# Optimization experiments

Hardware: AMD Instinct MI355X
Metric: run time of the kernel (lower is better)

The kernel has to match this reference:

```python
import jax, jax.numpy as jnp
import numpy as np

B, L, H = 32, 512, 1024
H2 = H // 2          # split half = 512
D_ATTN = 64
EPS = 1e-5


def setup_inputs() -> dict:
    key = jax.random.key(0)
    ks = jax.random.split(key, 6)
    x = jax.random.normal(ks[0], (B, L, H), dtype=jnp.float32)
    # LayerNorm params (default torch init: weight=1, bias=0)
    ln_gamma = jnp.ones((H2,), jnp.float32)
    ln_beta = jnp.zeros((H2,), jnp.float32)
    # Toeplitz params (module inits w_vector=0, bias=1; use small random w for nontrivial math)
    w_vector = jax.random.normal(ks[1], (2 * L - 1,), jnp.float32) * 0.02
    t_bias = jnp.ones((L,), jnp.float32)
    # TinyAttention: kqv Linear(H2 -> 3*d_attn), proj Linear(d_attn -> H2)
    kqv_w = jax.random.normal(ks[2], (H2, 3 * D_ATTN), jnp.float32) * 0.02
    kqv_b = jnp.zeros((3 * D_ATTN,), jnp.float32)
    proj_w = jax.random.normal(ks[3], (D_ATTN, H2), jnp.float32) * 0.02
    proj_b = jnp.zeros((H2,), jnp.float32)
    return {"x": x, "ln_gamma": ln_gamma, "ln_beta": ln_beta,
            "w_vector": w_vector, "t_bias": t_bias,
            "kqv_w": kqv_w, "kqv_b": kqv_b, "proj_w": proj_w, "proj_b": proj_b}


def _toeplitz(w_vector):
    # Faithful replication of get_toeplitz(): pad, tile, trim, reshape, crop.
    r = w_vector.shape[0] // 2            # = L - 1
    t = jnp.pad(w_vector, (0, L))         # length 3L - 1
    t = jnp.tile(t, L)[:-L]               # length L * (3L - 2)
    t = t.reshape(L, 3 * L - 2)
    return t[:, r:-r]                      # [L, L]


def _tiny_attention(v, kqv_w, kqv_b, proj_w, proj_b):
    kqv = v @ kqv_w + kqv_b                        # [B, L, 3*d_attn]
    k, q, val = jnp.split(kqv, 3, axis=-1)         # chunk order: key, query, value
    scale = 1.0 / jnp.sqrt(jnp.float32(q.shape[-1]))
    scores = jnp.einsum('bqd,bkd->bqk', q, k) * scale
    soft = jax.nn.softmax(scores, axis=-1)
    head = jnp.einsum('bqk,bkd->bqd', soft, val)   # [B, L, d_attn]
    return head @ proj_w + proj_b                  # [B, L, H2]


def reference(x, ln_gamma, ln_beta, w_vector, t_bias, kqv_w, kqv_b, proj_w, proj_b):
    u, v = jnp.split(x, 2, axis=-1)                # each [B, L, H2]
    head = _tiny_attention(v, kqv_w, kqv_b, proj_w, proj_b)
    # LayerNorm over last dim
    mu = jnp.mean(v, axis=-1, keepdims=True)
    var = jnp.mean(jnp.square(v - mu), axis=-1, keepdims=True)
    vn = (v - mu) * jax.lax.rsqrt(var + EPS) * ln_gamma + ln_beta
    # spatial (Toeplitz) mixing: permute -> [B, H2, L], matmul [L, L], bias
    w_t = _toeplitz(w_vector)
    vm = jnp.einsum('blc,lm->bmc', vn, w_t.T).transpose(0, 2, 1)  # keep faithful: vp @ w_t
    vm = jnp.einsum('bcl,lm->bcm', vn.transpose(0, 2, 1), w_t) + t_bias
    v_out = vm.transpose(0, 2, 1) + head           # [B, L, H2]
    return u * v_out
```

## Files before the change

kernel.cpp:

```cpp
#include <hip/hip_runtime.h>
#include <math.h>

#define NB 32
#define LL 512
#define HH 1024
#define H2 512
#define DA 64

typedef unsigned int u32;
typedef unsigned short u16;
typedef __bf16 bf16x8 __attribute__((ext_vector_type(8)));
typedef float f32x4 __attribute__((ext_vector_type(4)));

__device__ __forceinline__ u16 f2bu(float f) {
    u32 u = __builtin_bit_cast(u32, f);
    u = (u + 0x7fff + ((u >> 16) & 1)) >> 16;
    return (u16)u;
}

__device__ __forceinline__ void async_cp16(const void* g, void* l) {
    __builtin_amdgcn_global_load_lds(
        (const __attribute__((address_space(1))) u32*)g,
        (__attribute__((address_space(3))) u32*)l, 16, 0, 0);
}

__global__ void prep_kernel(const float* __restrict__ wv,
                            const float* __restrict__ kqvw,
                            const float* __restrict__ projw,
                            u16* __restrict__ wt, u16* __restrict__ kqvwT,
                            u16* __restrict__ projwT) {
    int e = blockIdx.x * 256 + threadIdx.x;
    if (e < 262144) {
        int m = e >> 9, l = e & 511;
        wt[e] = f2bu(wv[511 + m - l]);
    } else if (e < 262144 + 98304) {
        int i = e - 262144;
        int n = i >> 9, k = i & 511;
        kqvwT[i] = f2bu(kqvw[(size_t)k * 192 + n]);
    } else {
        int i = e - 360448;
        int c = i >> 6, d = i & 63;
        projwT[i] = f2bu(projw[(size_t)d * 512 + c]);
    }
}

__global__ void ln_kernel(const float* __restrict__ x,
                          const float* __restrict__ gamma,
                          const float* __restrict__ beta,
                          u16* __restrict__ vn) {
    int row = blockIdx.x;
    const float* vr = x + (size_t)row * HH + H2;
    int t = threadIdx.x;
    float a0 = vr[t], a1 = vr[t + 256];
    float s = a0 + a1, ss = a0 * a0 + a1 * a1;
#pragma unroll
    for (int off = 32; off > 0; off >>= 1) {
        s  += __shfl_down(s, off);
        ss += __shfl_down(ss, off);
    }
    __shared__ float ws[4], wss[4], stats[2];
    int wave = t >> 6;
    if ((t & 63) == 0) { ws[wave] = s; wss[wave] = ss; }
    __syncthreads();
    if (t == 0) {
        float S  = ws[0] + ws[1] + ws[2] + ws[3];
        float SS = wss[0] + wss[1] + wss[2] + wss[3];
        float mu  = S * (1.0f / H2);
        float var = SS * (1.0f / H2) - mu * mu;
        stats[0] = mu; stats[1] = rsqrtf(var + 1e-5f);
    }
    __syncthreads();
    float mu = stats[0], rstd = stats[1];
    u16* o = vn + (size_t)row * H2;
    o[t]       = f2bu((a0 - mu) * rstd * gamma[t]       + beta[t]);
    o[t + 256] = f2bu((a1 - mu) * rstd * gamma[t + 256] + beta[t + 256]);
}

__global__ void transpose_kernel(const u16* __restrict__ in, u16* __restrict__ outT) {
    __shared__ u16 T[64][65];
    int b = blockIdx.z, l0 = blockIdx.y * 64, c0 = blockIdx.x * 64;
    int t = threadIdx.x;
#pragma unroll
    for (int s = 0; s < 4; ++s) {
        int ci = t + s * 256;
        int row = ci >> 4, c4 = (ci & 15) * 4;
        ushort4 v = *(const ushort4*)(in + ((size_t)(b * LL + l0 + row)) * H2 + c0 + c4);
        T[c4 + 0][row] = v.x; T[c4 + 1][row] = v.y;
        T[c4 + 2][row] = v.z; T[c4 + 3][row] = v.w;
    }
    __syncthreads();
#pragma unroll
    for (int s = 0; s < 4; ++s) {
        int ci = t + s * 256;
        int c = ci >> 4, l4 = (ci & 15) * 4;
        ushort4 w;
        w.x = T[c][l4 + 0]; w.y = T[c][l4 + 1];
        w.z = T[c][l4 + 2]; w.w = T[c][l4 + 3];
        *(ushort4*)(outT + ((size_t)(b * H2 + c0 + c)) * LL + l0 + l4) = w;
    }
}

__global__ __launch_bounds__(256, 2)
void kqv_kernel(const float* __restrict__ x, const u16* __restrict__ wT,
                const float* __restrict__ bias,
                u16* __restrict__ qb, u16* __restrict__ kb, u16* __restrict__ vT) {
    __shared__ u16 smem[8192];
    u16* As = smem;
    u16* Bs = smem + 2048;
    int r0 = blockIdx.x * 64;
    int t = threadIdx.x, lane = t & 63, wid = t >> 6;
    int wm = (wid >> 1) * 32, wn = (wid & 1) * 96;
    int l15 = lane & 15, q16 = lane >> 4, q8 = q16 * 8;
    f32x4 acc[2][6] = {};
    for (int k0 = 0; k0 < 512; k0 += 32) {
#pragma unroll
        for (int s = 0; s < 3; ++s) {
            int ci = t + s * 256;
            async_cp16(wT + (size_t)(ci >> 2) * 512 + k0 + (ci & 3) * 8, Bs + ci * 8);
        }
#pragma unroll
        for (int s = 0; s < 2; ++s) {
            int ci = t + s * 256;
            int row = ci >> 3, c4 = (ci & 7) * 4;
            float4 v = *(const float4*)(x + (size_t)(r0 + row) * HH + H2 + k0 + c4);
            ushort4 p;
            p.x = f2bu(v.x); p.y = f2bu(v.y); p.z = f2bu(v.z); p.w = f2bu(v.w);
            *(ushort4*)(As + row * 32 + c4) = p;
        }
        __syncthreads();
        bf16x8 a[2], bb[6];
#pragma unroll
        for (int i = 0; i < 2; ++i)
            a[i] = *(const bf16x8*)(As + (wm + i * 16 + l15) * 32 + q8);
#pragma unroll
        for (int j = 0; j < 6; ++j)
            bb[j] = *(const bf16x8*)(Bs + (wn + j * 16 + l15) * 32 + q8);
#pragma unroll
        for (int i = 0; i < 2; ++i)
#pragma unroll
            for (int j = 0; j < 6; ++j)
                acc[i][j] = __builtin_amdgcn_mfma_f32_16x16x32_bf16(a[i], bb[j], acc[i][j], 0, 0, 0);
        __syncthreads();
    }
    u16* Ts = smem;
    int bb2 = r0 >> 9, l0loc = r0 & 511;
    int rq = q16 * 4;
#pragma unroll
    for (int i = 0; i < 2; ++i)
#pragma unroll
        for (int r = 0; r < 4; ++r) {
            int mloc = wm + i * 16 + rq + r;
            size_t mg = (size_t)(r0 + mloc);
#pragma unroll
            for (int j = 0; j < 6; ++j) {
                int n = wn + j * 16 + l15;
                u16 hv = f2bu(acc[i][j][r] + bias[n]);
                if (n < 64)       kb[mg * 64 + n] = hv;
                else if (n < 128) qb[mg * 64 + (n - 64)] = hv;
                else              Ts[(n - 128) * 68 + mloc] = hv;
            }
        }
    __syncthreads();
    int d = t >> 2, mo = (t & 3) * 16;
    u16* dst = vT + ((size_t)(bb2 * 64 + d)) * 512 + l0loc + mo;
    const u16* srcl = Ts + d * 68 + mo;
#pragma unroll
    for (int c = 0; c < 4; ++c)
        ((ushort4*)dst)[c] = ((const ushort4*)srcl)[c];
}

#define VLD 136
__global__ __launch_bounds__(256, 4)
void attn_kernel(const u16* __restrict__ qb, const u16* __restrict__ kb,
                 const u16* __restrict__ vT, u16* __restrict__ head) {
    __shared__ u16 Ps[4 * 16 * VLD];
    __shared__ float Osh[4][16 * 65];
    __shared__ float Msh[4][16], Lsh[4][16];
    int b = blockIdx.y, q0 = blockIdx.x * 16;
    int t = threadIdx.x, lane = t & 63, w = t >> 6;
    int l15 = lane & 15, q16 = lane >> 4, q8 = q16 * 8;
    int kc = w * 128;
    const u16* qg = qb + (size_t)b * LL * DA;
    const u16* kg = kb + (size_t)b * LL * DA;
    const u16* vg = vT + (size_t)b * DA * LL;

    bf16x8 aq[2];
#pragma unroll
    for (int s = 0; s < 2; ++s)
        aq[s] = *(const bf16x8*)(qg + (size_t)(q0 + l15) * DA + s * 32 + q8);

    f32x4 sc[8] = {};
#pragma unroll
    for (int j = 0; j < 8; ++j) {
#pragma unroll
        for (int s = 0; s < 2; ++s) {
            bf16x8 bk = *(const bf16x8*)(kg + (size_t)(kc + j * 16 + l15) * DA + s * 32 + q8);
            sc[j] = __builtin_amdgcn_mfma_f32_16x16x32_bf16(aq[s], bk, sc[j], 0, 0, 0);
        }
    }
    float mx[4], sm[4];
#pragma unroll
    for (int j = 0; j < 8; ++j)
#pragma unroll
        for (int r = 0; r < 4; ++r) sc[j][r] *= 0.125f;
#pragma unroll
    for (int r = 0; r < 4; ++r) {
        float m0 = sc[0][r];
#pragma unroll
        for (int j = 1; j < 8; ++j) m0 = fmaxf(m0, sc[j][r]);
        m0 = fmaxf(m0, __shfl_xor(m0, 1));
        m0 = fmaxf(m0, __shfl_xor(m0, 2));
        m0 = fmaxf(m0, __shfl_xor(m0, 4));
        m0 = fmaxf(m0, __shfl_xor(m0, 8));
        mx[r] = m0;
    }
#pragma unroll
    for (int j = 0; j < 8; ++j)
#pragma unroll
        for (int r = 0; r < 4; ++r) sc[j][r] = __expf(sc[j][r] - mx[r]);
#pragma unroll
    for (int r = 0; r < 4; ++r) {
        float s0 = sc[0][r];
#pragma unroll
        for (int j = 1; j < 8; ++j) s0 += sc[j][r];
        s0 += __shfl_xor(s0, 1);
        s0 += __shfl_xor(s0, 2);
        s0 += __shfl_xor(s0, 4);
        s0 += __shfl_xor(s0, 8);
        sm[r] = s0;
    }
    u16* Pw = Ps + w * 16 * VLD;
#pragma unroll
    for (int j = 0; j < 8; ++j)
#pragma unroll
        for (int r = 0; r < 4; ++r)
            Pw[(q16 * 4 + r) * VLD + j * 16 + l15] = f2bu(sc[j][r]);
    f32x4 o[4] = {};
#pragma unroll
    for (int kt = 0; kt < 4; ++kt) {
        bf16x8 ap = *(const bf16x8*)(Pw + l15 * VLD + kt * 32 + q8);
#pragma unroll
        for (int j = 0; j < 4; ++j) {
            bf16x8 bv = *(const bf16x8*)(vg + (size_t)(j * 16 + l15) * LL + kc + kt * 32 + q8);
            o[j] = __builtin_amdgcn_mfma_f32_16x16x32_bf16(ap, bv, o[j], 0, 0, 0);
        }
    }
#pragma unroll
    for (int j = 0; j < 4; ++j)
#pragma unroll
        for (int r = 0; r < 4; ++r)
            Osh[w][(q16 * 4 + r) * 65 + j * 16 + l15] = o[j][r];
    if (l15 == 0) {
#pragma unroll
        for (int r = 0; r < 4; ++r) {
            Msh[w][q16 * 4 + r] = mx[r];
            Lsh[w][q16 * 4 + r] = sm[r];
        }
    }
    __syncthreads();
    int q = t >> 4, dg = (t & 15) * 4;
    float m0 = Msh[0][q], m1 = Msh[1][q], m2 = Msh[2][q], m3 = Msh[3][q];
    float ms = fmaxf(fmaxf(m0, m1), fmaxf(m2, m3));
    float f0 = __expf(m0 - ms), f1 = __expf(m1 - ms), f2 = __expf(m2 - ms), f3 = __expf(m3 - ms);
    float lst = Lsh[0][q] * f0 + Lsh[1][q] * f1 + Lsh[2][q] * f2 + Lsh[3][q] * f3;
    float inv = 1.0f / lst;
    ushort4 res;
    u16* rp = (u16*)&res;
#pragma unroll
    for (int i = 0; i < 4; ++i) {
        int idx = q * 65 + dg + i;
        float a = Osh[0][idx] * f0 + Osh[1][idx] * f1 + Osh[2][idx] * f2 + Osh[3][idx] * f3;
        rp[i] = f2bu(a * inv);
    }
    *(ushort4*)(head + (size_t)(b * LL + q0 + q) * DA + dg) = res;
}

__device__ __forceinline__ void mfma_step(const u16* As, const u16* Bs,
                                          f32x4 acc[4][4], int wm, int wn, int lane) {
    int l15 = lane & 15, q8 = (lane >> 4) * 8;
    bf16x8 a[4], bv[4];
#pragma unroll
    for (int i = 0; i < 4; ++i)
        a[i] = *(const bf16x8*)(As + (wm + i * 16 + l15) * 32 + q8);
#pragma unroll
    for (int j = 0; j < 4; ++j)
        bv[j] = *(const bf16x8*)(Bs + (wn + j * 16 + l15) * 32 + q8);
#pragma unroll
    for (int i = 0; i < 4; ++i)
#pragma unroll
        for (int j = 0; j < 4; ++j)
            acc[i][j] = __builtin_amdgcn_mfma_f32_16x16x32_bf16(a[i], bv[j], acc[i][j], 0, 0, 0);
}

__global__ __launch_bounds__(256, 2)
void mix_kernel(const u16* __restrict__ wt,
                const u16* __restrict__ vnT,
                const u16* __restrict__ headb,
                const u16* __restrict__ projwT,
                const float* __restrict__ x,
                const float* __restrict__ tbias,
                const float* __restrict__ projb,
                float* __restrict__ out) {
    __shared__ u16 As[128 * 32];
    __shared__ u16 Bs[128 * 32];
    int b = blockIdx.z, m0 = blockIdx.y * 128, c0 = blockIdx.x * 128;
    int t = threadIdx.x, lane = t & 63, wid = t >> 6;
    int wm = (wid >> 1) * 64, wn = (wid & 1) * 64;
    f32x4 acc[4][4] = {};
    int ci0 = t, ci1 = t + 256;
    int r0a = ci0 >> 2, s0a = (ci0 & 3) * 8;
    int r1a = ci1 >> 2, s1a = (ci1 & 3) * 8;
    const u16* Ag = wt + (size_t)m0 * 512;
    const u16* Bg = vnT + ((size_t)b * H2 + c0) * 512;
    for (int k0 = 0; k0 < 512; k0 += 32) {
        async_cp16(Ag + (size_t)r0a * 512 + k0 + s0a, As + ci0 * 8);
        async_cp16(Ag + (size_t)r1a * 512 + k0 + s1a, As + ci1 * 8);
        async_cp16(Bg + (size_t)r0a * 512 + k0 + s0a, Bs + ci0 * 8);
        async_cp16(Bg + (size_t)r1a * 512 + k0 + s1a, Bs + ci1 * 8);
        __syncthreads();
        mfma_step(As, Bs, acc, wm, wn, lane);
        __syncthreads();
    }
    const u16* Hg = headb + ((size_t)b * LL + m0) * DA;
    const u16* Pg = projwT + (size_t)c0 * DA;
    for (int k0 = 0; k0 < 64; k0 += 32) {
        async_cp16(Hg + (size_t)r0a * 64 + k0 + s0a, As + ci0 * 8);
        async_cp16(Hg + (size_t)r1a * 64 + k0 + s1a, As + ci1 * 8);
        async_cp16(Pg + (size_t)r0a * 64 + k0 + s0a, Bs + ci0 * 8);
        async_cp16(Pg + (size_t)r1a * 64 + k0 + s1a, Bs + ci1 * 8);
        __syncthreads();
        mfma_step(As, Bs, acc, wm, wn, lane);
        __syncthreads();
    }
    int l15 = lane & 15, rq = (lane >> 4) * 4;
#pragma unroll
    for (int i = 0; i < 4; ++i) {
#pragma unroll
        for (int r = 0; r < 4; ++r) {
            int m = m0 + wm + i * 16 + rq + r;
            float tb = tbias[m];
            const float* xrow = x + ((size_t)b * LL + m) * HH;
            float* orow = out + ((size_t)b * LL + m) * H2;
#pragma unroll
            for (int j = 0; j < 4; ++j) {
                int c = c0 + wn + j * 16 + l15;
                float val = acc[i][j][r] + tb + projb[c];
                orow[c] = xrow[c] * val;
            }
        }
    }
}

extern "C" void kernel_launch(void* const* d_in, const int* in_sizes, int n_in,
                              void* d_out, int out_size, void* d_ws, size_t ws_size,
                              hipStream_t stream) {
    (void)in_sizes; (void)n_in; (void)out_size; (void)ws_size;
    const float* x     = (const float*)d_in[0];
    const float* gamma = (const float*)d_in[1];
    const float* beta  = (const float*)d_in[2];
    const float* wv    = (const float*)d_in[3];
    const float* tb    = (const float*)d_in[4];
    const float* kqvw  = (const float*)d_in[5];
    const float* kqvb  = (const float*)d_in[6];
    const float* projw = (const float*)d_in[7];
    const float* projb = (const float*)d_in[8];
    float* out = (float*)d_out;

    u16* vn_bf   = (u16*)d_ws;
    u16* vnT_bf  = vn_bf + (size_t)NB * LL * H2;
    u16* qb      = vnT_bf + (size_t)NB * LL * H2;
    u16* kb      = qb + (size_t)NB * LL * DA;
    u16* vTb     = kb + (size_t)NB * LL * DA;
    u16* head_bf = vTb + (size_t)NB * LL * DA;
    u16* wt_bf   = head_bf + (size_t)NB * LL * DA;
    u16* kqvwT   = wt_bf + 512 * 512;
    u16* projwT  = kqvwT + 192 * 512;

    prep_kernel     <<<1536, 256, 0, stream>>>(wv, kqvw, projw, wt_bf, kqvwT, projwT);
    ln_kernel       <<<NB * LL, 256, 0, stream>>>(x, gamma, beta, vn_bf);
    transpose_kernel<<<dim3(8, 8, NB), 256, 0, stream>>>(vn_bf, vnT_bf);
    kqv_kernel      <<<NB * LL / 64, 256, 0, stream>>>(x, kqvwT, kqvb, qb, kb, vTb);
    attn_kernel     <<<dim3(32, NB), 256, 0, stream>>>(qb, kb, vTb, head_bf);
    mix_kernel      <<<dim3(4, 4, NB), 256, 0, stream>>>(wt_bf, vnT_bf, head_bf, projwT, x, tb, projb, out);
}
```

Measured before the change: 192.7 us.

## Fuse weight prep, LayerNorm and transpose; swizzle LDS and widen K tiles in GEMMs

```diff
diff --git a/kernel.cpp b/kernel.cpp
--- a/kernel.cpp
+++ b/kernel.cpp
@@ -24,79 +24,65 @@
         (__attribute__((address_space(3))) u32*)l, 16, 0, 0);
 }
 
-__global__ void prep_kernel(const float* __restrict__ wv,
-                            const float* __restrict__ kqvw,
-                            const float* __restrict__ projw,
-                            u16* __restrict__ wt, u16* __restrict__ kqvwT,
-                            u16* __restrict__ projwT) {
-    int e = blockIdx.x * 256 + threadIdx.x;
-    if (e < 262144) {
-        int m = e >> 9, l = e & 511;
-        wt[e] = f2bu(wv[511 + m - l]);
-    } else if (e < 262144 + 98304) {
-        int i = e - 262144;
-        int n = i >> 9, k = i & 511;
-        kqvwT[i] = f2bu(kqvw[(size_t)k * 192 + n]);
-    } else {
-        int i = e - 360448;
-        int c = i >> 6, d = i & 63;
-        projwT[i] = f2bu(projw[(size_t)d * 512 + c]);
-    }
-}
-
-__global__ void ln_kernel(const float* __restrict__ x,
-                          const float* __restrict__ gamma,
-                          const float* __restrict__ beta,
-                          u16* __restrict__ vn) {
-    int row = blockIdx.x;
-    const float* vr = x + (size_t)row * HH + H2;
-    int t = threadIdx.x;
-    float a0 = vr[t], a1 = vr[t + 256];
-    float s = a0 + a1, ss = a0 * a0 + a1 * a1;
-#pragma unroll
-    for (int off = 32; off > 0; off >>= 1) {
-        s  += __shfl_down(s, off);
-        ss += __shfl_down(ss, off);
-    }
-    __shared__ float ws[4], wss[4], stats[2];
-    int wave = t >> 6;
-    if ((t & 63) == 0) { ws[wave] = s; wss[wave] = ss; }
-    __syncthreads();
-    if (t == 0) {
-        float S  = ws[0] + ws[1] + ws[2] + ws[3];
-        float SS = wss[0] + wss[1] + wss[2] + wss[3];
-        float mu  = S * (1.0f / H2);
-        float var = SS * (1.0f / H2) - mu * mu;
-        stats[0] = mu; stats[1] = rsqrtf(var + 1e-5f);
-    }
-    __syncthreads();
-    float mu = stats[0], rstd = stats[1];
-    u16* o = vn + (size_t)row * H2;
-    o[t]       = f2bu((a0 - mu) * rstd * gamma[t]       + beta[t]);
-    o[t + 256] = f2bu((a1 - mu) * rstd * gamma[t + 256] + beta[t + 256]);
-}
-
-__global__ void transpose_kernel(const u16* __restrict__ in, u16* __restrict__ outT) {
-    __shared__ u16 T[64][65];
-    int b = blockIdx.z, l0 = blockIdx.y * 64, c0 = blockIdx.x * 64;
-    int t = threadIdx.x;
-#pragma unroll
-    for (int s = 0; s < 4; ++s) {
-        int ci = t + s * 256;
-        int row = ci >> 4, c4 = (ci & 15) * 4;
-        ushort4 v = *(const ushort4*)(in + ((size_t)(b * LL + l0 + row)) * H2 + c0 + c4);
-        T[c4 + 0][row] = v.x; T[c4 + 1][row] = v.y;
-        T[c4 + 2][row] = v.z; T[c4 + 3][row] = v.w;
-    }
-    __syncthreads();
-#pragma unroll
-    for (int s = 0; s < 4; ++s) {
-        int ci = t + s * 256;
-        int c = ci >> 4, l4 = (ci & 15) * 4;
-        ushort4 w;
-        w.x = T[c][l4 + 0]; w.y = T[c][l4 + 1];
-        w.z = T[c][l4 + 2]; w.w = T[c][l4 + 3];
-        *(ushort4*)(outT + ((size_t)(b * H2 + c0 + c)) * LL + l0 + l4) = w;
+__global__ __launch_bounds__(256, 2)
+void ln_t_kernel(const float* __restrict__ x,
+                 const float* __restrict__ gamma, const float* __restrict__ beta,
+                 const float* __restrict__ wv, const float* __restrict__ kqvw,
+                 const float* __restrict__ projw,
+                 u16* __restrict__ vnT, u16* __restrict__ wt,
+                 u16* __restrict__ kqvwT, u16* __restrict__ projwT) {
+    __shared__ u16 T[64 * 68];
+    int blk = blockIdx.x, t = threadIdx.x;
+#pragma unroll
+    for (int s = 0; s < 6; ++s) {
+        int e = blk * 1536 + s * 256 + t;
+        if (e < 262144) {
+            int m = e >> 9, l = e & 511;
+            wt[e] = f2bu(wv[511 + m - l]);
+        } else if (e < 262144 + 98304) {
+            int i = e - 262144;
+            int n = i >> 9, k = i & 511;
+            kqvwT[i] = f2bu(kqvw[(size_t)k * 192 + n]);
+        } else {
+            int i = e - 360448;
+            int c = i >> 6, d = i & 63;
+            projwT[i] = f2bu(projw[(size_t)d * 512 + c]);
+        }
+    }
+    int b = blk >> 3, l0 = (blk & 7) * 64;
+    int r = t >> 2, q = t & 3;
+    const float* xr = x + ((size_t)(b * LL + l0 + r)) * HH + H2;
+    float s1 = 0.0f, s2 = 0.0f;
+#pragma unroll
+    for (int i = 0; i < 32; ++i) {
+        float4 v = *(const float4*)(xr + q * 128 + i * 4);
+        s1 += v.x + v.y + v.z + v.w;
+        s2 += v.x * v.x + v.y * v.y + v.z * v.z + v.w * v.w;
+    }
+    s1 += __shfl_xor(s1, 1); s2 += __shfl_xor(s2, 1);
+    s1 += __shfl_xor(s1, 2); s2 += __shfl_xor(s2, 2);
+    float mu = s1 * (1.0f / H2);
+    float rstd = rsqrtf(s2 * (1.0f / H2) - mu * mu + 1e-5f);
+    for (int ct = 0; ct < 8; ++ct) {
+        int cb = (t & 3) * 16;
+#pragma unroll
+        for (int i = 0; i < 4; ++i) {
+            float4 v = *(const float4*)(xr + ct * 64 + cb + i * 4);
+            int c = cb + i * 4;
+            T[(c + 0) * 68 + r] = f2bu((v.x - mu) * rstd * gamma[ct * 64 + c + 0] + beta[ct * 64 + c + 0]);
+            T[(c + 1) * 68 + r] = f2bu((v.y - mu) * rstd * gamma[ct * 64 + c + 1] + beta[ct * 64 + c + 1]);
+            T[(c + 2) * 68 + r] = f2bu((v.z - mu) * rstd * gamma[ct * 64 + c + 2] + beta[ct * 64 + c + 2]);
+            T[(c + 3) * 68 + r] = f2bu((v.w - mu) * rstd * gamma[ct * 64 + c + 3] + beta[ct * 64 + c + 3]);
+        }
+        __syncthreads();
+        int c = t >> 2, lo = (t & 3) * 16;
+        u16* dst = vnT + ((size_t)(b * H2 + ct * 64 + c)) * LL + l0 + lo;
+        const u16* src = T + c * 68 + lo;
+        ((ushort4*)dst)[0] = ((const ushort4*)src)[0];
+        ((ushort4*)dst)[1] = ((const ushort4*)src)[1];
+        ((ushort4*)dst)[2] = ((const ushort4*)src)[2];
+        ((ushort4*)dst)[3] = ((const ushort4*)src)[3];
+        __syncthreads();
     }
 }
 
@@ -104,69 +90,65 @@
 void kqv_kernel(const float* __restrict__ x, const u16* __restrict__ wT,
                 const float* __restrict__ bias,
                 u16* __restrict__ qb, u16* __restrict__ kb, u16* __restrict__ vT) {
-    __shared__ u16 smem[8192];
-    u16* As = smem;
-    u16* Bs = smem + 2048;
-    int r0 = blockIdx.x * 64;
+    __shared__ u16 As[32 * 72];
+    __shared__ u16 Bs[192 * 64];
+    u16* Ts = As;
+    int r0 = blockIdx.x * 32;
     int t = threadIdx.x, lane = t & 63, wid = t >> 6;
-    int wm = (wid >> 1) * 32, wn = (wid & 1) * 96;
-    int l15 = lane & 15, q16 = lane >> 4, q8 = q16 * 8;
-    f32x4 acc[2][6] = {};
-    for (int k0 = 0; k0 < 512; k0 += 32) {
-#pragma unroll
-        for (int s = 0; s < 3; ++s) {
+    int wm = (wid & 1) * 16, wn = (wid >> 1) * 96;
+    int l15 = lane & 15, q16 = lane >> 4, q8 = q16 * 8, s7 = l15 & 7;
+    f32x4 acc[6] = {};
+    for (int k0 = 0; k0 < 512; k0 += 64) {
+#pragma unroll
+        for (int s = 0; s < 6; ++s) {
             int ci = t + s * 256;
-            async_cp16(wT + (size_t)(ci >> 2) * 512 + k0 + (ci & 3) * 8, Bs + ci * 8);
+            int grow = ci >> 3, gcol = ((ci & 7) ^ (grow & 7)) << 3;
+            async_cp16(wT + (size_t)grow * 512 + k0 + gcol, Bs + ci * 8);
         }
 #pragma unroll
         for (int s = 0; s < 2; ++s) {
             int ci = t + s * 256;
-            int row = ci >> 3, c4 = (ci & 7) * 4;
+            int row = ci >> 4, c4 = (ci & 15) * 4;
             float4 v = *(const float4*)(x + (size_t)(r0 + row) * HH + H2 + k0 + c4);
             ushort4 p;
             p.x = f2bu(v.x); p.y = f2bu(v.y); p.z = f2bu(v.z); p.w = f2bu(v.w);
-            *(ushort4*)(As + row * 32 + c4) = p;
-        }
-        __syncthreads();
-        bf16x8 a[2], bb[6];
-#pragma unroll
-        for (int i = 0; i < 2; ++i)
-            a[i] = *(const bf16x8*)(As + (wm + i * 16 + l15) * 32 + q8);
-#pragma unroll
-        for (int j = 0; j < 6; ++j)
-            bb[j] = *(const bf16x8*)(Bs + (wn + j * 16 + l15) * 32 + q8);
-#pragma unroll
-        for (int i = 0; i < 2; ++i)
-#pragma unroll
-            for (int j = 0; j < 6; ++j)
-                acc[i][j] = __builtin_amdgcn_mfma_f32_16x16x32_bf16(a[i], bb[j], acc[i][j], 0, 0, 0);
-        __syncthreads();
-    }
-    u16* Ts = smem;
-    int bb2 = r0 >> 9, l0loc = r0 & 511;
-    int rq = q16 * 4;
-#pragma unroll
-    for (int i = 0; i < 2; ++i)
-#pragma unroll
-        for (int r = 0; r < 4; ++r) {
-            int mloc = wm + i * 16 + rq + r;
-            size_t mg = (size_t)(r0 + mloc);
+            *(ushort4*)(As + row * 72 + c4) = p;
+        }
+        __syncthreads();
+#pragma unroll
+        for (int kk = 0; kk < 2; ++kk) {
+            int j0 = kk * 4 + q16;
+            bf16x8 a = *(const bf16x8*)(As + (wm + l15) * 72 + kk * 32 + q8);
 #pragma unroll
             for (int j = 0; j < 6; ++j) {
                 int n = wn + j * 16 + l15;
-                u16 hv = f2bu(acc[i][j][r] + bias[n]);
-                if (n < 64)       kb[mg * 64 + n] = hv;
-                else if (n < 128) qb[mg * 64 + (n - 64)] = hv;
-                else              Ts[(n - 128) * 68 + mloc] = hv;
+                bf16x8 bb = *(const bf16x8*)(Bs + (n * 8 + (j0 ^ (n & 7))) * 8);
+                acc[j] = __builtin_amdgcn_mfma_f32_16x16x32_bf16(a, bb, acc[j], 0, 0, 0);
             }
         }
+        __syncthreads();
+    }
+    int bidx = blockIdx.x >> 4, l0loc = (blockIdx.x & 15) * 32;
+    int rq = q16 * 4;
+#pragma unroll
+    for (int r = 0; r < 4; ++r) {
+        int mloc = wm + rq + r;
+        size_t mg = (size_t)(r0 + mloc);
+#pragma unroll
+        for (int j = 0; j < 6; ++j) {
+            int n = wn + j * 16 + l15;
+            u16 hv = f2bu(acc[j][r] + bias[n]);
+            if (n < 64)       kb[mg * 64 + n] = hv;
+            else if (n < 128) qb[mg * 64 + (n - 64)] = hv;
+            else              Ts[(n - 128) * 36 + mloc] = hv;
+        }
+    }
     __syncthreads();
-    int d = t >> 2, mo = (t & 3) * 16;
-    u16* dst = vT + ((size_t)(bb2 * 64 + d)) * 512 + l0loc + mo;
-    const u16* srcl = Ts + d * 68 + mo;
-#pragma unroll
-    for (int c = 0; c < 4; ++c)
-        ((ushort4*)dst)[c] = ((const ushort4*)srcl)[c];
+    int d = t >> 2, lo = (t & 3) * 8;
+    u16* dst = vT + ((size_t)(bidx * 64 + d)) * 512 + l0loc + lo;
+    const u16* src = Ts + d * 36 + lo;
+    ((ushort4*)dst)[0] = ((const ushort4*)src)[0];
+    ((ushort4*)dst)[1] = ((const ushort4*)src)[1];
 }
 
 #define VLD 136
@@ -258,38 +240,47 @@
         }
     }
     __syncthreads();
-    int q = t >> 4, dg = (t & 15) * 4;
-    float m0 = Msh[0][q], m1 = Msh[1][q], m2 = Msh[2][q], m3 = Msh[3][q];
+    int qq = t >> 4, dg = (t & 15) * 4;
+    float m0 = Msh[0][qq], m1 = Msh[1][qq], m2 = Msh[2][qq], m3 = Msh[3][qq];
     float ms = fmaxf(fmaxf(m0, m1), fmaxf(m2, m3));
     float f0 = __expf(m0 - ms), f1 = __expf(m1 - ms), f2 = __expf(m2 - ms), f3 = __expf(m3 - ms);
-    float lst = Lsh[0][q] * f0 + Lsh[1][q] * f1 + Lsh[2][q] * f2 + Lsh[3][q] * f3;
+    float lst = Lsh[0][qq] * f0 + Lsh[1][qq] * f1 + Lsh[2][qq] * f2 + Lsh[3][qq] * f3;
     float inv = 1.0f / lst;
     ushort4 res;
     u16* rp = (u16*)&res;
 #pragma unroll
     for (int i = 0; i < 4; ++i) {
-        int idx = q * 65 + dg + i;
+        int idx = qq * 65 + dg + i;
         float a = Osh[0][idx] * f0 + Osh[1][idx] * f1 + Osh[2][idx] * f2 + Osh[3][idx] * f3;
         rp[i] = f2bu(a * inv);
     }
-    *(ushort4*)(head + (size_t)(b * LL + q0 + q) * DA + dg) = res;
-}
-
-__device__ __forceinline__ void mfma_step(const u16* As, const u16* Bs,
-                                          f32x4 acc[4][4], int wm, int wn, int lane) {
-    int l15 = lane & 15, q8 = (lane >> 4) * 8;
-    bf16x8 a[4], bv[4];
-#pragma unroll
-    for (int i = 0; i < 4; ++i)
-        a[i] = *(const bf16x8*)(As + (wm + i * 16 + l15) * 32 + q8);
-#pragma unroll
-    for (int j = 0; j < 4; ++j)
-        bv[j] = *(const bf16x8*)(Bs + (wn + j * 16 + l15) * 32 + q8);
-#pragma unroll
-    for (int i = 0; i < 4; ++i)
-#pragma unroll
-        for (int j = 0; j < 4; ++j)
-            acc[i][j] = __builtin_amdgcn_mfma_f32_16x16x32_bf16(a[i], bv[j], acc[i][j], 0, 0, 0);
+    *(ushort4*)(head + (size_t)(b * LL + q0 + qq) * DA + dg) = res;
+}
+
+__device__ __forceinline__ void mfma_tile64(const u16* As, const u16* Bs,
+                                            f32x4 acc[4][4], int wm, int wn,
+                                            int l15, int q16) {
+    int s7 = l15 & 7;
+#pragma unroll
+    for (int kk = 0; kk < 2; ++kk) {
+        int j0 = kk * 4 + q16;
+        bf16x8 a[4], bv[4];
+#pragma unroll
+        for (int i = 0; i < 4; ++i) {
+            int row = wm + i * 16 + l15;
+            a[i] = *(const bf16x8*)(As + (row * 8 + (j0 ^ s7)) * 8);
+        }
+#pragma unroll
+        for (int j = 0; j < 4; ++j) {
+            int row = wn + j * 16 + l15;
+            bv[j] = *(const bf16x8*)(Bs + (row * 8 + (j0 ^ s7)) * 8);
+        }
+#pragma unroll
+        for (int i = 0; i < 4; ++i)
+#pragma unroll
+            for (int j = 0; j < 4; ++j)
+                acc[i][j] = __builtin_amdgcn_mfma_f32_16x16x32_bf16(a[i], bv[j], acc[i][j], 0, 0, 0);
+    }
 }
 
 __global__ __launch_bounds__(256, 2)
@@ -301,38 +292,42 @@
                 const float* __restrict__ tbias,
                 const float* __restrict__ projb,
                 float* __restrict__ out) {
-    __shared__ u16 As[128 * 32];
-    __shared__ u16 Bs[128 * 32];
+    __shared__ u16 As[128 * 64];
+    __shared__ u16 Bs[128 * 64];
     int b = blockIdx.z, m0 = blockIdx.y * 128, c0 = blockIdx.x * 128;
     int t = threadIdx.x, lane = t & 63, wid = t >> 6;
     int wm = (wid >> 1) * 64, wn = (wid & 1) * 64;
+    int l15 = lane & 15, q16 = lane >> 4;
     f32x4 acc[4][4] = {};
-    int ci0 = t, ci1 = t + 256;
-    int r0a = ci0 >> 2, s0a = (ci0 & 3) * 8;
-    int r1a = ci1 >> 2, s1a = (ci1 & 3) * 8;
     const u16* Ag = wt + (size_t)m0 * 512;
     const u16* Bg = vnT + ((size_t)b * H2 + c0) * 512;
-    for (int k0 = 0; k0 < 512; k0 += 32) {
-        async_cp16(Ag + (size_t)r0a * 512 + k0 + s0a, As + ci0 * 8);
-        async_cp16(Ag + (size_t)r1a * 512 + k0 + s1a, As + ci1 * 8);
-        async_cp16(Bg + (size_t)r0a * 512 + k0 + s0a, Bs + ci0 * 8);
-        async_cp16(Bg + (size_t)r1a * 512 + k0 + s1a, Bs + ci1 * 8);
-        __syncthreads();
-        mfma_step(As, Bs, acc, wm, wn, lane);
-        __syncthreads();
-    }
-    const u16* Hg = headb + ((size_t)b * LL + m0) * DA;
-    const u16* Pg = projwT + (size_t)c0 * DA;
-    for (int k0 = 0; k0 < 64; k0 += 32) {
-        async_cp16(Hg + (size_t)r0a * 64 + k0 + s0a, As + ci0 * 8);
-        async_cp16(Hg + (size_t)r1a * 64 + k0 + s1a, As + ci1 * 8);
-        async_cp16(Pg + (size_t)r0a * 64 + k0 + s0a, Bs + ci0 * 8);
-        async_cp16(Pg + (size_t)r1a * 64 + k0 + s1a, Bs + ci1 * 8);
-        __syncthreads();
-        mfma_step(As, Bs, acc, wm, wn, lane);
-        __syncthreads();
-    }
-    int l15 = lane & 15, rq = (lane >> 4) * 4;
+    for (int k0 = 0; k0 < 512; k0 += 64) {
+#pragma unroll
+        for (int s = 0; s < 4; ++s) {
+            int ci = t + s * 256;
+            int grow = ci >> 3, gcol = ((ci & 7) ^ (grow & 7)) << 3;
+            async_cp16(Ag + (size_t)grow * 512 + k0 + gcol, As + ci * 8);
+            async_cp16(Bg + (size_t)grow * 512 + k0 + gcol, Bs + ci * 8);
+        }
+        __syncthreads();
+        mfma_tile64(As, Bs, acc, wm, wn, l15, q16);
+        __syncthreads();
+    }
+    {
+        const u16* Hg = headb + ((size_t)b * LL + m0) * DA;
+        const u16* Pg = projwT + (size_t)c0 * DA;
+#pragma unroll
+        for (int s = 0; s < 4; ++s) {
+            int ci = t + s * 256;
+            int grow = ci >> 3, gcol = ((ci & 7) ^ (grow & 7)) << 3;
+            async_cp16(Hg + (size_t)grow * 64 + gcol, As + ci * 8);
+            async_cp16(Pg + (size_t)grow * 64 + gcol, Bs + ci * 8);
+        }
+        __syncthreads();
+        mfma_tile64(As, Bs, acc, wm, wn, l15, q16);
+        __syncthreads();
+    }
+    int rq = q16 * 4;
 #pragma unroll
     for (int i = 0; i < 4; ++i) {
 #pragma unroll
@@ -366,8 +361,7 @@
     const float* projb = (const float*)d_in[8];
     float* out = (float*)d_out;
 
-    u16* vn_bf   = (u16*)d_ws;
-    u16* vnT_bf  = vn_bf + (size_t)NB * LL * H2;
+    u16* vnT_bf  = (u16*)d_ws;
     u16* qb      = vnT_bf + (size_t)NB * LL * H2;
     u16* kb      = qb + (size_t)NB * LL * DA;
     u16* vTb     = kb + (size_t)NB * LL * DA;
@@ -376,10 +370,10 @@
     u16* kqvwT   = wt_bf + 512 * 512;
     u16* projwT  = kqvwT + 192 * 512;
 
-    prep_kernel     <<<1536, 256, 0, stream>>>(wv, kqvw, projw, wt_bf, kqvwT, projwT);
-    ln_kernel       <<<NB * LL, 256, 0, stream>>>(x, gamma, beta, vn_bf);
-    transpose_kernel<<<dim3(8, 8, NB), 256, 0, stream>>>(vn_bf, vnT_bf);
-    kqv_kernel      <<<NB * LL / 64, 256, 0, stream>>>(x, kqvwT, kqvb, qb, kb, vTb);
-    attn_kernel     <<<dim3(32, NB), 256, 0, stream>>>(qb, kb, vTb, head_bf);
-    mix_kernel      <<<dim3(4, 4, NB), 256, 0, stream>>>(wt_bf, vnT_bf, head_bf, projwT, x, tb, projb, out);
-}
+    ln_t_kernel<<<256, 256, 0, stream>>>(x, gamma, beta, wv, kqvw, projw,
+                                         vnT_bf, wt_bf, kqvwT, projwT);
+    kqv_kernel <<<NB * LL / 32, 256, 0, stream>>>(x, kqvwT, kqvb, qb, kb, vTb);
+    attn_kernel<<<dim3(32, NB), 256, 0, stream>>>(qb, kb, vTb, head_bf);
+    mix_kernel <<<dim3(4, 4, NB), 256, 0, stream>>>(wt_bf, vnT_bf, head_bf, projwT,
+                                                    x, tb, projb, out);
+}
```

New measurement: 183.4 us. 1.05x faster.
